# Optimization experiments

Measured on AMD Instinct MI355X. Metric: run time of the kernel, lower is better.

The kernel has to match this reference:

```python
import jax, jax.numpy as jnp
import numpy as np

EMBED = 768
HEAD = 64

def setup_inputs() -> dict:
    key = jax.random.key(0)
    k1, k2, k3, k4 = jax.random.split(key, 4)
    x = jax.random.normal(k1, (8, 2048, EMBED), dtype=jnp.float32)
    # torch nn.Linear weights: [out, in], applied as x @ W.T
    scale = 1.0 / np.sqrt(EMBED)
    Wq = jax.random.uniform(k2, (HEAD, EMBED), jnp.float32, -scale, scale)
    Wk = jax.random.uniform(k3, (HEAD, EMBED), jnp.float32, -scale, scale)
    Wv = jax.random.uniform(k4, (HEAD, EMBED), jnp.float32, -scale, scale)
    return {"x": x, "Wq": Wq, "Wk": Wk, "Wv": Wv}

def reference(x, Wq, Wk, Wv):
    B, S, E = x.shape
    q = jnp.einsum('bse,he->bsh', x, Wq)
    k = jnp.einsum('bse,he->bsh', x, Wk)
    v = jnp.einsum('bse,he->bsh', x, Wv)
    # NOTE: faithful to source: weights / embed**(-0.5) == weights * sqrt(embed)
    scores = jnp.einsum('bqh,bkh->bqk', q, k) * jnp.sqrt(jnp.float32(E))
    causal = jnp.tril(jnp.ones((S, S), dtype=bool))
    scores = jnp.where(causal, scores, -jnp.inf)
    attn = jax.nn.softmax(scores, axis=-1)
    return jnp.einsum('bqk,bkh->bqh', attn, v)
```

## Files before the change

kernel.cpp:

```cpp
#include <hip/hip_runtime.h>
#include <math.h>

#define EMBED 768
#define SEQ   2048
#define NB    8
#define QSCALE 39.98113776623437f

typedef short  short4v __attribute__((ext_vector_type(4)));
typedef short  short8 __attribute__((ext_vector_type(8)));
typedef float  f32x4  __attribute__((ext_vector_type(4)));
typedef float  f32x16 __attribute__((ext_vector_type(16)));
typedef unsigned int uint2v __attribute__((ext_vector_type(2)));

#define WHI_OFF  0u
#define WLO_OFF  147456u
#define QHI_OFF  294912u
#define QLO_OFF  (294912u + 1u*1048576u)
#define KHI_OFF  (294912u + 2u*1048576u)
#define KLO_OFF  (294912u + 3u*1048576u)
#define VT_OFF   (294912u + 4u*1048576u)
#define FLT_BASE 2768896u

__device__ __forceinline__ ushort f2bf(float f) {
    unsigned u = __float_as_uint(f);
    return (ushort)((u + 0x7FFFu + ((u >> 16) & 1u)) >> 16);
}
__device__ __forceinline__ ushort f2bf_trunc(float f) {
    return (ushort)(__float_as_uint(f) >> 16);
}
__device__ __forceinline__ float bf2f(ushort h) {
    return __uint_as_float(((unsigned)h) << 16);
}
__device__ __forceinline__ uint cvtpk(float a, float b) {
    uint r;
    asm("v_cvt_pk_bf16_f32 %0, %1, %2" : "=v"(r) : "v"(a), "v"(b));
    return r;
}

union U8 { uint u[4]; short8 s; };

__global__ __launch_bounds__(256)
void split_w_kernel(const float* __restrict__ Wq, const float* __restrict__ Wk,
                    const float* __restrict__ Wv,
                    ushort* __restrict__ w_hi, ushort* __restrict__ w_lo)
{
    int idx = blockIdx.x * 256 + threadIdx.x;
    if (idx >= 192 * EMBED) return;
    int row = idx / EMBED, e = idx - row * EMBED;
    float f;
    if (row < 64)       f = Wq[row * EMBED + e] * QSCALE;
    else if (row < 128) f = Wk[(row - 64) * EMBED + e];
    else                f = Wv[(row - 128) * EMBED + e];
    ushort hi = f2bf(f);
    w_hi[idx] = hi;
    w_lo[idx] = f2bf_trunc(f - bf2f(hi));
}

__global__ __launch_bounds__(512)
void proj_kernel(const float* __restrict__ x,
                 const ushort* __restrict__ w_hi, const ushort* __restrict__ w_lo,
                 ushort* __restrict__ q_hi, ushort* __restrict__ q_lo,
                 ushort* __restrict__ k_hi, ushort* __restrict__ k_lo,
                 ushort* __restrict__ v_t)
{
    __shared__ __align__(16) ushort xah[2][64][72], xal[2][64][72];
    __shared__ __align__(16) ushort wbh[2][192][72];
    __shared__ __align__(16) ushort wbl[2][128][72];

    const int t    = threadIdx.x;
    const int lane = t & 63;
    const int wid  = t >> 6;
    const int wm   = wid >> 2;
    const int wn   = wid & 3;
    const int ln   = lane & 15;
    const int kg   = lane >> 4;
    const int row0 = blockIdx.x * 64;

#define LOADSET(e0, XR0, XR1, WH0, WH1, WH2, WL0, WL1) do {                       \
        const float* xp_ = x + (size_t)(row0 + (t >> 4)) * EMBED + (e0) + (t & 15) * 4; \
        XR0 = *(const float4*)xp_;                                                \
        XR1 = *(const float4*)(xp_ + 32 * EMBED);                                 \
        const ushort* wp_ = w_hi + (size_t)(t >> 3) * EMBED + (e0) + (t & 7) * 8; \
        WH0 = *(const short8*)wp_;                                                \
        WH1 = *(const short8*)(wp_ + 64 * EMBED);                                 \
        WH2 = *(const short8*)(wp_ + 128 * EMBED);                                \
        const ushort* lp_ = w_lo + (size_t)(t >> 3) * EMBED + (e0) + (t & 7) * 8; \
        WL0 = *(const short8*)lp_;                                                \
        WL1 = *(const short8*)(lp_ + 64 * EMBED);                                 \
    } while (0)

#define STORESET(BUF, XR0, XR1, WH0, WH1, WH2, WL0, WL1) do {                     \
        const int xr_ = t >> 4, xc_ = (t & 15) * 4;                               \
        const float f0_[4] = {XR0.x, XR0.y, XR0.z, XR0.w};                        \
        const float f1_[4] = {XR1.x, XR1.y, XR1.z, XR1.w};                        \
        short4v h0_, l0_, h1_, l1_;                                               \
        _Pragma("unroll")                                                         \
        for (int i_ = 0; i_ < 4; ++i_) {                                          \
            ushort h_ = f2bf(f0_[i_]);                                            \
            h0_[i_] = (short)h_;                                                  \
            l0_[i_] = (short)f2bf_trunc(f0_[i_] - bf2f(h_));                      \
        }                                                                         \
        _Pragma("unroll")                                                         \
        for (int i_ = 0; i_ < 4; ++i_) {                                          \
            ushort h_ = f2bf(f1_[i_]);                                            \
            h1_[i_] = (short)h_;                                                  \
            l1_[i_] = (short)f2bf_trunc(f1_[i_] - bf2f(h_));                      \
        }                                                                         \
        *(short4v*)&xah[BUF][xr_][xc_]      = h0_;                                \
        *(short4v*)&xal[BUF][xr_][xc_]      = l0_;                                \
        *(short4v*)&xah[BUF][xr_ + 32][xc_] = h1_;                                \
        *(short4v*)&xal[BUF][xr_ + 32][xc_] = l1_;                                \
        const int wr_ = t >> 3, wc_ = (t & 7) * 8;                                \
        *(short8*)&wbh[BUF][wr_][wc_]       = WH0;                                \
        *(short8*)&wbh[BUF][wr_ + 64][wc_]  = WH1;                                \
        *(short8*)&wbh[BUF][wr_ + 128][wc_] = WH2;                                \
        *(short8*)&wbl[BUF][wr_][wc_]       = WL0;                                \
        *(short8*)&wbl[BUF][wr_ + 64][wc_]  = WL1;                                \
    } while (0)

#define COMPUTE(BUF) do {                                                         \
        short8 ah_[2][2], al_[2][2];                                              \
        _Pragma("unroll")                                                         \
        for (int mt_ = 0; mt_ < 2; ++mt_)                                         \
            _Pragma("unroll")                                                     \
            for (int ks_ = 0; ks_ < 2; ++ks_) {                                   \
                ah_[mt_][ks_] = *(const short8*)&xah[BUF][wm * 32 + mt_ * 16 + ln][ks_ * 32 + kg * 8]; \
                al_[mt_][ks_] = *(const short8*)&xal[BUF][wm * 32 + mt_ * 16 + ln][ks_ * 32 + kg * 8]; \
            }                                                                     \
        _Pragma("unroll")                                                         \
        for (int j_ = 0; j_ < 3; ++j_) {                                          \
            const int ntg_ = j_ * 4 + wn;                                         \
            _Pragma("unroll")                                                     \
            for (int ks_ = 0; ks_ < 2; ++ks_) {                                   \
                const int co_ = ks_ * 32 + kg * 8;                                \
                short8 bh_ = *(const short8*)&wbh[BUF][ntg_ * 16 + ln][co_];      \
                _Pragma("unroll")                                                 \
                for (int mt_ = 0; mt_ < 2; ++mt_)                                 \
                    acc[mt_][j_] = __builtin_amdgcn_mfma_f32_16x16x32_bf16(ah_[mt_][ks_], bh_, acc[mt_][j_], 0, 0, 0); \
                if (j_ < 2) {                                                     \
                    short8 bl_ = *(const short8*)&wbl[BUF][ntg_ * 16 + ln][co_];  \
                    _Pragma("unroll")                                             \
                    for (int mt_ = 0; mt_ < 2; ++mt_) {                           \
                        acc[mt_][j_] = __builtin_amdgcn_mfma_f32_16x16x32_bf16(ah_[mt_][ks_], bl_, acc[mt_][j_], 0, 0, 0); \
                        acc[mt_][j_] = __builtin_amdgcn_mfma_f32_16x16x32_bf16(al_[mt_][ks_], bh_, acc[mt_][j_], 0, 0, 0); \
                    }                                                             \
                }                                                                 \
            }                                                                     \
        }                                                                         \
    } while (0)

    const f32x4 vzero = {0.f, 0.f, 0.f, 0.f};
    f32x4 acc[2][3];
#pragma unroll
    for (int mt = 0; mt < 2; ++mt)
#pragma unroll
        for (int j = 0; j < 3; ++j) acc[mt][j] = vzero;

    float4 xrA0, xrA1; short8 whA0, whA1, whA2, wlA0, wlA1;
    float4 xrB0, xrB1; short8 whB0, whB1, whB2, wlB0, wlB1;
    float4 xrC0, xrC1; short8 whC0, whC1, whC2, wlC0, wlC1;

    LOADSET(0,   xrA0, xrA1, whA0, whA1, whA2, wlA0, wlA1);
    LOADSET(64,  xrB0, xrB1, whB0, whB1, whB2, wlB0, wlB1);
    LOADSET(128, xrC0, xrC1, whC0, whC1, whC2, wlC0, wlC1);

#define ITER(C_, VMC, BUF, X0, X1, W0, W1, W2, L0, L1) do {                       \
        asm volatile("s_waitcnt vmcnt(" #VMC ")" ::: "memory");                   \
        STORESET(BUF, X0, X1, W0, W1, W2, L0, L1);                                \
        asm volatile("s_waitcnt lgkmcnt(0)" ::: "memory");                        \
        __builtin_amdgcn_s_barrier();                                             \
        if ((C_) + 3 < 12) LOADSET(((C_) + 3) * 64, X0, X1, W0, W1, W2, L0, L1);  \
        COMPUTE(BUF);                                                             \
    } while (0)

    ITER(0,  14, 0, xrA0, xrA1, whA0, whA1, whA2, wlA0, wlA1);
    ITER(1,  14, 1, xrB0, xrB1, whB0, whB1, whB2, wlB0, wlB1);
    ITER(2,  14, 0, xrC0, xrC1, whC0, whC1, whC2, wlC0, wlC1);
    ITER(3,  14, 1, xrA0, xrA1, whA0, whA1, whA2, wlA0, wlA1);
    ITER(4,  14, 0, xrB0, xrB1, whB0, whB1, whB2, wlB0, wlB1);
    ITER(5,  14, 1, xrC0, xrC1, whC0, whC1, whC2, wlC0, wlC1);
    ITER(6,  14, 0, xrA0, xrA1, whA0, whA1, whA2, wlA0, wlA1);
    ITER(7,  14, 1, xrB0, xrB1, whB0, whB1, whB2, wlB0, wlB1);
    ITER(8,  14, 0, xrC0, xrC1, whC0, whC1, whC2, wlC0, wlC1);
    ITER(9,  14, 1, xrA0, xrA1, whA0, whA1, whA2, wlA0, wlA1);
    ITER(10,  7, 0, xrB0, xrB1, whB0, whB1, whB2, wlB0, wlB1);
    ITER(11,  0, 1, xrC0, xrC1, whC0, whC1, whC2, wlC0, wlC1);
#undef ITER
#undef LOADSET
#undef STORESET
#undef COMPUTE

#pragma unroll
    for (int mt = 0; mt < 2; ++mt) {
        const int rbase = row0 + wm * 32 + mt * 16 + kg * 4;
#pragma unroll
        for (int j = 0; j < 3; ++j) {
            const int col = (j * 4 + wn) * 16 + ln;
#pragma unroll
            for (int r = 0; r < 4; ++r) {
                int rg = rbase + r;
                int b = rg >> 11, s = rg & 2047;
                size_t rowoff = ((size_t)b * SEQ + s) * 64;
                float val = acc[mt][j][r];
                if (col < 64) {
                    ushort h = f2bf(val);
                    q_hi[rowoff + col] = h;
                    q_lo[rowoff + col] = f2bf_trunc(val - bf2f(h));
                } else if (col < 128) {
                    ushort h = f2bf(val);
                    k_hi[rowoff + (col - 64)] = h;
                    k_lo[rowoff + (col - 64)] = f2bf_trunc(val - bf2f(h));
                } else {
                    v_t[((size_t)b * 64 + (col - 128)) * SEQ + s] = f2bf(val);
                }
            }
        }
    }
}

__global__ __launch_bounds__(256)
void attn_kernel(const ushort* __restrict__ q_hi, const ushort* __restrict__ q_lo,
                 const ushort* __restrict__ k_hi, const ushort* __restrict__ k_lo,
                 const ushort* __restrict__ v_t,
                 float* __restrict__ oP, float* __restrict__ mP,
                 float* __restrict__ lP, int Z)
{
    __shared__ __align__(16) ushort kv[3][3][64][64];

    const int t    = threadIdx.x;
    const int lane = t & 63;
    const int w    = t >> 6;
    const int l31  = lane & 31;
    const int h8   = (lane >> 5) << 3;
    const int sw   = (lane & 7) << 3;
    const int b    = blockIdx.x & 7;
    const int pr   = (blockIdx.x >> 3) & 7;
    const int z    = blockIdx.x >> 6;
    const int qA   = 15 - pr;
    const int qB   = pr;
    const int cA   = 2 * qA + 2;
    const int T    = 34;

    const ushort* qhb = q_hi + (size_t)b * SEQ * 64;
    const ushort* qlb = q_lo + (size_t)b * SEQ * 64;
    const ushort* khb = k_hi + (size_t)b * SEQ * 64;
    const ushort* klb = k_lo + (size_t)b * SEQ * 64;
    const ushort* vtb = v_t + (size_t)b * 64 * SEQ;
    float* oPz = oP + (size_t)z * 1048576u;
    float* mPz = mP + (size_t)z * 16384u;
    float* lPz = lP + (size_t)z * 16384u;

    const int srow8 = lane >> 3;
    const int scol  = ((lane & 7) << 3) ^ ((lane >> 3) << 3);

    auto stage = [&](int g, int cbuf) {
        const int kk = (g < cA) ? g : g - cA;
        const int j0 = kk << 6;
        ushort* base = &kv[cbuf][0][0][0];
#pragma unroll
        for (int s = 0; s < 6; ++s) {
            const int i = w * 6 + s;
            const int row = ((i & 7) << 3) + srow8;
            const ushort* gp;
            if (i < 8)       gp = khb + (size_t)(j0 + row) * 64 + scol;
            else if (i < 16) gp = klb + (size_t)(j0 + row) * 64 + scol;
            else             gp = vtb + (size_t)row * SEQ + j0 + scol;
            __builtin_amdgcn_global_load_lds(
                (const __attribute__((address_space(1))) void*)gp,
                (__attribute__((address_space(3))) void*)(base + i * 512),
                16, 0, 0);
        }
    };

    auto loadQ = [&](int qb, short8 (&qh)[4], short8 (&ql)[4]) {
#pragma unroll
        for (int ks = 0; ks < 4; ++ks) {
            size_t off = (size_t)(qb * 128 + w * 32 + l31) * 64 + ks * 16 + h8;
            qh[ks] = *(const short8*)(qhb + off);
            ql[ks] = *(const short8*)(qlb + off);
        }
    };

    auto body = [&](int kk, int qb, f32x16 (&o)[2], float& m_run, float& l_run,
                    short8 (&qh)[4], short8 (&ql)[4], int cbuf) {
        const ushort* K0 = &kv[cbuf][0][0][0];
        const ushort* K1 = &kv[cbuf][1][0][0];
        const ushort* VT = &kv[cbuf][2][0][0];

        f32x16 sacc[2];
#pragma unroll
        for (int i = 0; i < 16; ++i) { sacc[0][i] = 0.f; sacc[1][i] = 0.f; }
        __builtin_amdgcn_s_setprio(1);
#pragma unroll
        for (int kt = 0; kt < 2; ++kt) {
            const int rb = (kt * 32 + l31) * 64;
#pragma unroll
            for (int ks = 0; ks < 4; ++ks) {
                const int c = (ks * 16 + h8) ^ sw;
                short8 ah = *(const short8*)(K0 + rb + c);
                short8 al = *(const short8*)(K1 + rb + c);
                sacc[kt] = __builtin_amdgcn_mfma_f32_32x32x16_bf16(ah, qh[ks], sacc[kt], 0, 0, 0);
                sacc[kt] = __builtin_amdgcn_mfma_f32_32x32x16_bf16(ah, ql[ks], sacc[kt], 0, 0, 0);
                sacc[kt] = __builtin_amdgcn_mfma_f32_32x32x16_bf16(al, qh[ks], sacc[kt], 0, 0, 0);
            }
        }
        __builtin_amdgcn_s_setprio(0);

        if ((kk >> 1) == qb) {
            const int q   = qb * 128 + w * 32 + l31;
            const int hi4 = (lane >> 5) << 2;
#pragma unroll
            for (int kt = 0; kt < 2; ++kt) {
                const int kb = kk * 64 + kt * 32 + hi4;
#pragma unroll
                for (int reg = 0; reg < 16; ++reg) {
                    const int key = kb + (reg & 3) + 8 * (reg >> 2);
                    if (key > q) sacc[kt][reg] = -1e30f;
                }
            }
        }

        float t8[8];
#pragma unroll
        for (int j = 0; j < 8; ++j)
            t8[j] = fmaxf(fmaxf(sacc[0][2*j], sacc[0][2*j+1]),
                          fmaxf(sacc[1][2*j], sacc[1][2*j+1]));
        float mx = fmaxf(fmaxf(fmaxf(t8[0], t8[1]), fmaxf(t8[2], t8[3])),
                         fmaxf(fmaxf(t8[4], t8[5]), fmaxf(t8[6], t8[7])));
        mx = fmaxf(mx, __shfl_xor(mx, 32));
        float mn   = fmaxf(m_run, mx);
        float corr = exp2f(m_run - mn);
        float p[2][16];
        float lt = 0.f;
#pragma unroll
        for (int kt = 0; kt < 2; ++kt)
#pragma unroll
            for (int reg = 0; reg < 16; ++reg) {
                p[kt][reg] = exp2f(sacc[kt][reg] - mn);
                lt += p[kt][reg];
            }
        lt += __shfl_xor(lt, 32);
        m_run = mn;
        l_run = l_run * corr + lt;
        o[0] = o[0] * corr;
        o[1] = o[1] * corr;

#pragma unroll
        for (int kt = 0; kt < 2; ++kt) {
            uint pk[8];
#pragma unroll
            for (int j = 0; j < 8; ++j) pk[j] = cvtpk(p[kt][2*j], p[kt][2*j+1]);
            U8 f0, f1;
#if __has_builtin(__builtin_amdgcn_permlane32_swap)
            uint2v a0 = __builtin_amdgcn_permlane32_swap(pk[0], pk[2], false, false);
            uint2v b0 = __builtin_amdgcn_permlane32_swap(pk[1], pk[3], false, false);
            uint2v a1 = __builtin_amdgcn_permlane32_swap(pk[4], pk[6], false, false);
            uint2v b1 = __builtin_amdgcn_permlane32_swap(pk[5], pk[7], false, false);
            f0.u[0] = a0.x; f0.u[1] = b0.x; f0.u[2] = a0.y; f0.u[3] = b0.y;
            f1.u[0] = a1.x; f1.u[1] = b1.x; f1.u[2] = a1.y; f1.u[3] = b1.y;
#else
            const bool hiH = (lane >= 32);
            uint rx[8];
#pragma unroll
            for (int j = 0; j < 8; ++j) rx[j] = (uint)__shfl_xor((int)pk[j], 32);
            f0.u[0] = hiH ? rx[2] : pk[0];
            f0.u[1] = hiH ? rx[3] : pk[1];
            f0.u[2] = hiH ? pk[2] : rx[0];
            f0.u[3] = hiH ? pk[3] : rx[1];
            f1.u[0] = hiH ? rx[6] : pk[4];
            f1.u[1] = hiH ? rx[7] : pk[5];
            f1.u[2] = hiH ? pk[6] : rx[4];
            f1.u[3] = hiH ? pk[7] : rx[5];
#endif
            __builtin_amdgcn_s_setprio(1);
#pragma unroll
            for (int ht = 0; ht < 2; ++ht) {
                const int row = ht * 32 + l31;
#pragma unroll
                for (int s2 = 0; s2 < 2; ++s2) {
                    const int c = (kt * 32 + s2 * 16 + h8) ^ sw;
                    short8 av = *(const short8*)(VT + row * 64 + c);
                    o[ht] = __builtin_amdgcn_mfma_f32_32x32x16_bf16(
                                av, (s2 ? f1.s : f0.s), o[ht], 0, 0, 0);
                }
            }
            __builtin_amdgcn_s_setprio(0);
        }
    };

    auto storeP = [&](int qb, f32x16 (&o)[2], float m_run, float l_run) {
        const size_t rowq = (size_t)b * SEQ + qb * 128 + w * 32 + l31;
        const int hb = (lane >> 5) << 2;
        float* op = oPz + rowq * 64;
#pragma unroll
        for (int ht = 0; ht < 2; ++ht)
#pragma unroll
            for (int rq = 0; rq < 4; ++rq) {
                float4 v = make_float4(o[ht][4*rq], o[ht][4*rq+1],
                                       o[ht][4*rq+2], o[ht][4*rq+3]);
                *(float4*)(op + ht * 32 + rq * 8 + hb) = v;
            }
        if (lane < 32) { mPz[rowq] = m_run; lPz[rowq] = l_run; }
    };

    short8 qh[4], ql[4];
    f32x16 o[2];
    float m_run, l_run;

    const int cnt = (T - 1 - z) / Z + 1;
    stage(z, 0);
    stage(z + Z, 1);
    loadQ(qA, qh, ql);
#pragma unroll
    for (int i = 0; i < 16; ++i) { o[0][i] = 0.f; o[1][i] = 0.f; }
    m_run = -INFINITY; l_run = 0.f;
    bool inB = false;

    for (int i = 0; i < cnt; ++i) {
        const int g = z + i * Z;
        if (i + 1 < cnt) asm volatile("s_waitcnt vmcnt(6)" ::: "memory");
        else             asm volatile("s_waitcnt vmcnt(0)" ::: "memory");
        __builtin_amdgcn_s_barrier();
        if (i + 2 < cnt) stage(z + (i + 2) * Z, (i + 2) % 3);
        if (g >= cA && !inB) {
            storeP(qA, o, m_run, l_run);
            loadQ(qB, qh, ql);
#pragma unroll
            for (int j = 0; j < 16; ++j) { o[0][j] = 0.f; o[1][j] = 0.f; }
            m_run = -INFINITY; l_run = 0.f;
            inB = true;
        }
        body(g < cA ? g : g - cA, g < cA ? qA : qB, o, m_run, l_run, qh, ql, i % 3);
    }

    if (!inB) {
        storeP(qA, o, m_run, l_run);
        const size_t rowq = (size_t)b * SEQ + qB * 128 + w * 32 + l31;
        float* op = oPz + rowq * 64;
        const int hb = (lane >> 5) << 2;
        float4 zz = make_float4(0.f, 0.f, 0.f, 0.f);
#pragma unroll
        for (int ht = 0; ht < 2; ++ht)
#pragma unroll
            for (int rq = 0; rq < 4; ++rq)
                *(float4*)(op + ht * 32 + rq * 8 + hb) = zz;
        if (lane < 32) { mPz[rowq] = -INFINITY; lPz[rowq] = 0.f; }
    } else {
        storeP(qB, o, m_run, l_run);
    }
}

__global__ __launch_bounds__(256)
void merge_kernel(const float* __restrict__ oP, const float* __restrict__ mP,
                  const float* __restrict__ lP, float* __restrict__ out, int Z)
{
    int idx = blockIdx.x * 256 + threadIdx.x;
    int R  = idx >> 4;
    int h0 = (idx & 15) << 2;
    float M = -INFINITY;
    for (int zz = 0; zz < Z; ++zz) M = fmaxf(M, mP[zz * 16384 + R]);
    float L = 0.f;
    float4 acc = make_float4(0.f, 0.f, 0.f, 0.f);
    for (int zz = 0; zz < Z; ++zz) {
        float c = exp2f(mP[zz * 16384 + R] - M);
        L += lP[zz * 16384 + R] * c;
        float4 a = *(const float4*)(oP + (size_t)zz * 1048576u + (size_t)R * 64 + h0);
        acc.x += a.x * c; acc.y += a.y * c; acc.z += a.z * c; acc.w += a.w * c;
    }
    float inv = 1.0f / L;
    float4 r = make_float4(acc.x * inv, acc.y * inv, acc.z * inv, acc.w * inv);
    *(float4*)(out + (size_t)R * 64 + h0) = r;
}

extern "C" void kernel_launch(void* const* d_in, const int* in_sizes, int n_in,
                              void* d_out, int out_size, void* d_ws, size_t ws_size,
                              hipStream_t stream)
{
    const float* x  = (const float*)d_in[0];
    const float* Wq = (const float*)d_in[1];
    const float* Wk = (const float*)d_in[2];
    const float* Wv = (const float*)d_in[3];
    float* out = (float*)d_out;

    ushort* ws = (ushort*)d_ws;
    float*  wsf = (float*)d_ws;
    ushort* w_hi = ws + WHI_OFF;
    ushort* w_lo = ws + WLO_OFF;
    ushort* q_hi = ws + QHI_OFF;
    ushort* q_lo = ws + QLO_OFF;
    ushort* k_hi = ws + KHI_OFF;
    ushort* k_lo = ws + KLO_OFF;
    ushort* v_t  = ws + VT_OFF;

    const int Z = 4;
    float* oP = wsf + FLT_BASE;
    float* mP = oP + (size_t)Z * 1048576u;
    float* lP = mP + (size_t)Z * 16384u;

    split_w_kernel<<<dim3(576), dim3(256), 0, stream>>>(Wq, Wk, Wv, w_hi, w_lo);
    proj_kernel<<<dim3(256), dim3(512), 0, stream>>>(x, w_hi, w_lo,
                                                     q_hi, q_lo, k_hi, k_lo, v_t);
    attn_kernel<<<dim3(64 * Z), dim3(256), 0, stream>>>(q_hi, q_lo, k_hi, k_lo, v_t,
                                                        oP, mP, lP, Z);
    merge_kernel<<<dim3(1024), dim3(256), 0, stream>>>(oP, mP, lP, out, Z);
}
```

Baseline: 58.44 us.

## Store partial attention outputs in bf16 and double the key-split factor

Partial output accumulators written by the attention kernel are now packed to bf16 instead of fp32, which halves the partial-output traffic between the attention and merge kernels. The split count Z rises from 4 to 8, launching twice as many attention blocks so each processes fewer key tiles, which improves occupancy across the GPU's CUs. The trade-off is extra merge work, a larger workspace, and bf16 rounding error in the partial outputs before the fp32 merge.

Measured after the change: 55.58 us (median of 3 runs). -4.9%, faster.

```diff
diff --git a/kernel.cpp b/kernel.cpp
--- a/kernel.cpp
+++ b/kernel.cpp
@@ -19,7 +19,8 @@
 #define KHI_OFF  (294912u + 2u*1048576u)
 #define KLO_OFF  (294912u + 3u*1048576u)
 #define VT_OFF   (294912u + 4u*1048576u)
-#define FLT_BASE 2768896u
+#define OPU_OFF  5537792u
+#define MPL_OFF  (5537792u + 8u*1048576u)
 
 __device__ __forceinline__ ushort f2bf(float f) {
     unsigned u = __float_as_uint(f);
@@ -222,7 +223,7 @@
 void attn_kernel(const ushort* __restrict__ q_hi, const ushort* __restrict__ q_lo,
                  const ushort* __restrict__ k_hi, const ushort* __restrict__ k_lo,
                  const ushort* __restrict__ v_t,
-                 float* __restrict__ oP, float* __restrict__ mP,
+                 ushort* __restrict__ oP, float* __restrict__ mP,
                  float* __restrict__ lP, int Z)
 {
     __shared__ __align__(16) ushort kv[3][3][64][64];
@@ -246,9 +247,9 @@
     const ushort* khb = k_hi + (size_t)b * SEQ * 64;
     const ushort* klb = k_lo + (size_t)b * SEQ * 64;
     const ushort* vtb = v_t + (size_t)b * 64 * SEQ;
-    float* oPz = oP + (size_t)z * 1048576u;
-    float* mPz = mP + (size_t)z * 16384u;
-    float* lPz = lP + (size_t)z * 16384u;
+    ushort* oPz = oP + (size_t)z * 1048576u;
+    float*  mPz = mP + (size_t)z * 16384u;
+    float*  lPz = lP + (size_t)z * 16384u;
 
     const int srow8 = lane >> 3;
     const int scol  = ((lane & 7) << 3) ^ ((lane >> 3) << 3);
@@ -391,14 +392,15 @@
     auto storeP = [&](int qb, f32x16 (&o)[2], float m_run, float l_run) {
         const size_t rowq = (size_t)b * SEQ + qb * 128 + w * 32 + l31;
         const int hb = (lane >> 5) << 2;
-        float* op = oPz + rowq * 64;
+        ushort* op = oPz + rowq * 64;
 #pragma unroll
         for (int ht = 0; ht < 2; ++ht)
 #pragma unroll
             for (int rq = 0; rq < 4; ++rq) {
-                float4 v = make_float4(o[ht][4*rq], o[ht][4*rq+1],
-                                       o[ht][4*rq+2], o[ht][4*rq+3]);
-                *(float4*)(op + ht * 32 + rq * 8 + hb) = v;
+                uint u0 = cvtpk(o[ht][4*rq],     o[ht][4*rq + 1]);
+                uint u1 = cvtpk(o[ht][4*rq + 2], o[ht][4*rq + 3]);
+                *(uint*)(op + ht * 32 + rq * 8 + hb)     = u0;
+                *(uint*)(op + ht * 32 + rq * 8 + hb + 2) = u1;
             }
         if (lane < 32) { mPz[rowq] = m_run; lPz[rowq] = l_run; }
     };
@@ -436,14 +438,15 @@
     if (!inB) {
         storeP(qA, o, m_run, l_run);
         const size_t rowq = (size_t)b * SEQ + qB * 128 + w * 32 + l31;
-        float* op = oPz + rowq * 64;
+        ushort* op = oPz + rowq * 64;
         const int hb = (lane >> 5) << 2;
-        float4 zz = make_float4(0.f, 0.f, 0.f, 0.f);
 #pragma unroll
         for (int ht = 0; ht < 2; ++ht)
 #pragma unroll
-            for (int rq = 0; rq < 4; ++rq)
-                *(float4*)(op + ht * 32 + rq * 8 + hb) = zz;
+            for (int rq = 0; rq < 4; ++rq) {
+                *(uint*)(op + ht * 32 + rq * 8 + hb)     = 0u;
+                *(uint*)(op + ht * 32 + rq * 8 + hb + 2) = 0u;
+            }
         if (lane < 32) { mPz[rowq] = -INFINITY; lPz[rowq] = 0.f; }
     } else {
         storeP(qB, o, m_run, l_run);
@@ -451,7 +454,7 @@
 }
 
 __global__ __launch_bounds__(256)
-void merge_kernel(const float* __restrict__ oP, const float* __restrict__ mP,
+void merge_kernel(const ushort* __restrict__ oP, const float* __restrict__ mP,
                   const float* __restrict__ lP, float* __restrict__ out, int Z)
 {
     int idx = blockIdx.x * 256 + threadIdx.x;
@@ -464,8 +467,13 @@
     for (int zz = 0; zz < Z; ++zz) {
         float c = exp2f(mP[zz * 16384 + R] - M);
         L += lP[zz * 16384 + R] * c;
-        float4 a = *(const float4*)(oP + (size_t)zz * 1048576u + (size_t)R * 64 + h0);
-        acc.x += a.x * c; acc.y += a.y * c; acc.z += a.z * c; acc.w += a.w * c;
+        const ushort* op = oP + (size_t)zz * 1048576u + (size_t)R * 64 + h0;
+        uint u0 = *(const uint*)op;
+        uint u1 = *(const uint*)(op + 2);
+        acc.x += bf2f((ushort)(u0 & 0xFFFFu)) * c;
+        acc.y += bf2f((ushort)(u0 >> 16))     * c;
+        acc.z += bf2f((ushort)(u1 & 0xFFFFu)) * c;
+        acc.w += bf2f((ushort)(u1 >> 16))     * c;
     }
     float inv = 1.0f / L;
     float4 r = make_float4(acc.x * inv, acc.y * inv, acc.z * inv, acc.w * inv);
@@ -483,7 +491,6 @@
     float* out = (float*)d_out;
 
     ushort* ws = (ushort*)d_ws;
-    float*  wsf = (float*)d_ws;
     ushort* w_hi = ws + WHI_OFF;
     ushort* w_lo = ws + WLO_OFF;
     ushort* q_hi = ws + QHI_OFF;
@@ -492,10 +499,10 @@
     ushort* k_lo = ws + KLO_OFF;
     ushort* v_t  = ws + VT_OFF;
 
-    const int Z = 4;
-    float* oP = wsf + FLT_BASE;
-    float* mP = oP + (size_t)Z * 1048576u;
-    float* lP = mP + (size_t)Z * 16384u;
+    const int Z = 8;
+    ushort* oP = ws + OPU_OFF;
+    float*  mP = (float*)(ws + MPL_OFF);
+    float*  lP = mP + (size_t)Z * 16384u;
 
     split_w_kernel<<<dim3(576), dim3(256), 0, stream>>>(Wq, Wk, Wv, w_hi, w_lo);
     proj_kernel<<<dim3(256), dim3(512), 0, stream>>>(x, w_hi, w_lo,
```
